# Optimization experiments

Measured on AMD Instinct MI355X. Metric: run time of the kernel, lower is better.

Reference implementation:

```python
import jax, jax.numpy as jnp
import numpy as np

EPS = 1e-12
LAMDA = 1.0
MAX_ITER = 10


def setup_inputs() -> dict:
    key = jax.random.key(0)
    k1, k2 = jax.random.split(key)
    B, L1, L2, D = 64, 1024, 1024, 256
    x1 = jax.random.normal(k1, (B, L1, D), dtype=jnp.float32)
    x2 = jax.random.normal(k2, (B, L2, D), dtype=jnp.float32)
    return {"x1": x1, "x2": x2}


def _cos(x1, x2):
    # batched cosine similarity: [B, L1, L2]
    M = jnp.einsum('bik,bjk->bij', x1, x2)
    a = jnp.sqrt(jnp.sum(x1 * x1, axis=-1, keepdims=True))  # [B, L1, 1]
    b = jnp.sqrt(jnp.sum(x2 * x2, axis=-1, keepdims=True))  # [B, L2, 1]
    norm = a * jnp.swapaxes(b, 1, 2)                          # [B, L1, L2]
    return M / (norm + EPS)


def reference(x1, x2):
    B, L1, _ = x1.shape
    L2 = x2.shape[1]
    M = 1.0 - _cos(x1, x2)          # [B, L1, L2] cost matrix
    K = jnp.exp(-M * LAMDA)
    w1 = jnp.full((B, L1, 1), 1.0 / L1, dtype=x1.dtype)
    w2 = jnp.full((B, L2, 1), 1.0 / L2, dtype=x1.dtype)
    ui = jnp.ones((B, L1, 1), dtype=x1.dtype)
    vi = jnp.ones((B, L2, 1), dtype=x1.dtype)
    Kt = jnp.swapaxes(K, 1, 2)      # [B, L2, L1]

    def body(_, carry):
        ui, vi = carry
        vi = w2 / (jnp.matmul(Kt, ui) + EPS)
        ui = w1 / (jnp.matmul(K, vi) + EPS)
        return (ui, vi)

    ui, vi = jax.lax.fori_loop(0, MAX_ITER, body, (ui, vi))
    G = ui * K * jnp.swapaxes(vi, 1, 2)   # transport plan [B, L1, L2]
    G_max = jnp.max(G, axis=(-1, -2), keepdims=True)
    G_min = jnp.min(G, axis=(-1, -2), keepdims=True)
    G = (G - G_min) / (G_max - G_min + EPS)
    return G * M
```

## Files before the change

kernel.cpp:

```cpp
#include <hip/hip_runtime.h>
#include <hip/hip_bf16.h>


#define EPSV 1e-12f
#define W1 0.0009765625f

typedef short  short8 __attribute__((ext_vector_type(8)));
typedef float  f32x4  __attribute__((ext_vector_type(4)));
typedef _Float16 h8   __attribute__((ext_vector_type(8)));

__device__ __forceinline__ short8 ld_cvt8(const float* p) {
  float4 f0 = *(const float4*)p;
  float4 f1 = *(const float4*)(p + 4);
  float2 p0; p0.x = f0.x; p0.y = f0.y;
  float2 p1; p1.x = f0.z; p1.y = f0.w;
  float2 p2; p2.x = f1.x; p2.y = f1.y;
  float2 p3; p3.x = f1.z; p3.y = f1.w;
  __hip_bfloat162 h0 = __float22bfloat162_rn(p0);
  __hip_bfloat162 h1 = __float22bfloat162_rn(p1);
  __hip_bfloat162 h2 = __float22bfloat162_rn(p2);
  __hip_bfloat162 h3 = __float22bfloat162_rn(p3);
  short2 a = *(short2*)&h0, b = *(short2*)&h1, c = *(short2*)&h2, d = *(short2*)&h3;
  short8 r;
  r[0] = a.x; r[1] = a.y; r[2] = b.x; r[3] = b.y;
  r[4] = c.x; r[5] = c.y; r[6] = d.x; r[7] = d.y;
  return r;
}

__global__ __launch_bounds__(256) void diag_kernel(float* __restrict__ out,
                                                   float val, int n) {
  int stride = gridDim.x * 256;
  for (int i = blockIdx.x * 256 + threadIdx.x; i < n; i += stride) out[i] = val;
}

__global__ __launch_bounds__(256) void prep_kernel(
    const float* __restrict__ x1, const float* __restrict__ x2,
    float* __restrict__ n1, float* __restrict__ n2,
    unsigned* __restrict__ mm) {
  int t = threadIdx.x, bid = blockIdx.x;
  if (bid == 0 && t < 128) mm[t] = (t < 64) ? 0u : 0x7f800000u;
  int row = bid * 4 + (t >> 6);
  int lane = t & 63;
  const float* xp; float* np_;
  int r = row;
  if (row < 65536) { xp = x1; np_ = n1; }
  else { r = row - 65536; xp = x2; np_ = n2; }
  float4 v = ((const float4*)(xp + (size_t)r * 256))[lane];
  float s = v.x * v.x + v.y * v.y + v.z * v.z + v.w * v.w;
  #pragma unroll
  for (int off = 1; off < 64; off <<= 1) s += __shfl_xor(s, off, 64);
  if (lane == 0) np_[r] = sqrtf(s);
}

__global__ __launch_bounds__(256) void gemm_kernel(
    const float* __restrict__ x1, const float* __restrict__ x2,
    const float* __restrict__ n1, const float* __restrict__ n2,
    _Float16* __restrict__ Kh) {
  __shared__ __align__(16) unsigned short smem[2 * 128 * 64];
  unsigned short* As = smem;
  unsigned short* Bs = smem + 128 * 64;
  int bid = blockIdx.x;
  int b = bid >> 6, tile = bid & 63;
  int ti = (tile >> 3) << 7, tj = (tile & 7) << 7;
  int t = threadIdx.x, lane = t & 63, wave = t >> 6;
  int wr = (wave >> 1) << 6, wc = (wave & 1) << 6;
  const float* Ag = x1 + ((size_t)(b * 1024 + ti)) * 256;
  const float* Bg = x2 + ((size_t)(b * 1024 + tj)) * 256;

  f32x4 acc[4][4];
  f32x4 zero = {0.f, 0.f, 0.f, 0.f};
  #pragma unroll
  for (int m = 0; m < 4; ++m)
    #pragma unroll
    for (int n = 0; n < 4; ++n) acc[m][n] = zero;

  short8 ra[4], rb[4];
  #pragma unroll
  for (int c = 0; c < 4; ++c) {
    int ch = t + (c << 8); int row = ch >> 3, kg = ch & 7;
    ra[c] = ld_cvt8(Ag + row * 256 + kg * 8);
    rb[c] = ld_cvt8(Bg + row * 256 + kg * 8);
  }

  for (int k0 = 0; k0 < 4; ++k0) {
    __syncthreads();
    #pragma unroll
    for (int c = 0; c < 4; ++c) {
      int ch = t + (c << 8); int row = ch >> 3, kg = ch & 7;
      int kgs = kg ^ (row & 7);
      *(short8*)(As + row * 64 + kgs * 8) = ra[c];
      *(short8*)(Bs + row * 64 + kgs * 8) = rb[c];
    }
    __syncthreads();
    if (k0 < 3) {
      #pragma unroll
      for (int c = 0; c < 4; ++c) {
        int ch = t + (c << 8); int row = ch >> 3, kg = ch & 7;
        ra[c] = ld_cvt8(Ag + row * 256 + (k0 + 1) * 64 + kg * 8);
        rb[c] = ld_cvt8(Bg + row * 256 + (k0 + 1) * 64 + kg * 8);
      }
    }
    #pragma unroll
    for (int ks = 0; ks < 2; ++ks) {
      short8 af[4], bfr[4];
      #pragma unroll
      for (int m = 0; m < 4; ++m) {
        int row = wr + m * 16 + (lane & 15);
        int c16 = (ks << 2) + (lane >> 4);
        af[m] = *(const short8*)(As + row * 64 + ((c16 ^ (row & 7)) << 3));
      }
      #pragma unroll
      for (int n = 0; n < 4; ++n) {
        int row = wc + n * 16 + (lane & 15);
        int c16 = (ks << 2) + (lane >> 4);
        bfr[n] = *(const short8*)(Bs + row * 64 + ((c16 ^ (row & 7)) << 3));
      }
      #pragma unroll
      for (int m = 0; m < 4; ++m)
        #pragma unroll
        for (int n = 0; n < 4; ++n)
          acc[m][n] = __builtin_amdgcn_mfma_f32_16x16x32_bf16(af[m], bfr[n], acc[m][n], 0, 0, 0);
    }
  }
  __syncthreads();

  _Float16* Ct = (_Float16*)smem;
  float a1v[4][4], b2v[4];
  #pragma unroll
  for (int m = 0; m < 4; ++m)
    #pragma unroll
    for (int q = 0; q < 4; ++q)
      a1v[m][q] = n1[(size_t)b * 1024 + ti + wr + m * 16 + ((lane >> 4) << 2) + q];
  #pragma unroll
  for (int n = 0; n < 4; ++n)
    b2v[n] = n2[(size_t)b * 1024 + tj + wc + n * 16 + (lane & 15)];
  #pragma unroll
  for (int m = 0; m < 4; ++m)
    #pragma unroll
    for (int n = 0; n < 4; ++n)
      #pragma unroll
      for (int q = 0; q < 4; ++q) {
        int rl = wr + m * 16 + ((lane >> 4) << 2) + q;
        int cl = wc + n * 16 + (lane & 15);
        float cosv = acc[m][n][q] / (a1v[m][q] * b2v[n] + EPSV);
        Ct[rl * 128 + cl] = (_Float16)__expf(cosv - 1.0f);
      }
  __syncthreads();
  size_t kbase = ((size_t)b << 20);
  #pragma unroll
  for (int c2i = 0; c2i < 8; ++c2i) {
    int c2 = t + (c2i << 8);
    int row = c2 >> 4, seg = c2 & 15;
    *(float4*)(Kh + kbase + (size_t)(ti + row) * 1024 + tj + seg * 8) = ((const float4*)Ct)[c2];
  }
}

__global__ __launch_bounds__(512) void ktu0_kernel(
    const _Float16* __restrict__ Kh, _Float16* __restrict__ dst) {
  int bid = blockIdx.x;
  int b = bid >> 2, s = bid & 3;
  int t = threadIdx.x, lane = t & 63, w = t >> 6;
  __shared__ float plds[8][1024];
  float pacc[16];
  #pragma unroll
  for (int k = 0; k < 16; ++k) pacc[k] = 0.f;
  const _Float16* kp = Kh + ((size_t)b << 20) + (size_t)(s * 256 + w) * 1024 + lane * 8;
  #pragma unroll 2
  for (int it = 0; it < 32; ++it) {
    h8 k0 = *(const h8*)(kp + (size_t)it * 8192);
    h8 k1 = *(const h8*)(kp + (size_t)it * 8192 + 512);
    #pragma unroll
    for (int k = 0; k < 8; ++k) { pacc[k] += (float)k0[k]; pacc[8 + k] += (float)k1[k]; }
  }
  float4 v0 = {pacc[0], pacc[1], pacc[2], pacc[3]};
  float4 v1 = {pacc[4], pacc[5], pacc[6], pacc[7]};
  float4 v2 = {pacc[8], pacc[9], pacc[10], pacc[11]};
  float4 v3 = {pacc[12], pacc[13], pacc[14], pacc[15]};
  *(float4*)&plds[w][lane * 8] = v0;
  *(float4*)&plds[w][lane * 8 + 4] = v1;
  *(float4*)&plds[w][512 + lane * 8] = v2;
  *(float4*)&plds[w][512 + lane * 8 + 4] = v3;
  __syncthreads();
  #pragma unroll
  for (int p = 0; p < 2; ++p) {
    int col = (p << 9) + t;
    float sum = plds[0][col] + plds[1][col] + plds[2][col] + plds[3][col]
              + plds[4][col] + plds[5][col] + plds[6][col] + plds[7][col];
    dst[((size_t)b << 12) + (s << 10) + col] = (_Float16)sum;
  }
}

template<int FINAL>
__global__ __launch_bounds__(512) void fused_kernel(
    const _Float16* __restrict__ Kh, const _Float16* __restrict__ src,
    _Float16* __restrict__ dst, float* __restrict__ zb,
    unsigned* __restrict__ mm) {
  int bid = blockIdx.x;
  int b = bid >> 2, s = bid & 3;
  int t = threadIdx.x, lane = t & 63, w = t >> 6;
  __shared__ float sv[1024];
  __shared__ float plds[8][1024];
  __shared__ float red[16];
  #pragma unroll
  for (int p = 0; p < 2; ++p) {
    int col = (p << 9) + t;
    const _Float16* sp = src + ((size_t)b << 12) + col;
    float y = (float)sp[0] + (float)sp[1024] + (float)sp[2048] + (float)sp[3072];
    sv[col] = W1 / (y + EPSV);
  }
  __syncthreads();
  float svr[16];
  {
    float4 s0 = *(const float4*)&sv[lane * 8];
    float4 s1 = *(const float4*)&sv[lane * 8 + 4];
    float4 s2 = *(const float4*)&sv[512 + lane * 8];
    float4 s3 = *(const float4*)&sv[512 + lane * 8 + 4];
    svr[0] = s0.x;  svr[1] = s0.y;  svr[2]  = s0.z;  svr[3]  = s0.w;
    svr[4] = s1.x;  svr[5] = s1.y;  svr[6]  = s1.z;  svr[7]  = s1.w;
    svr[8] = s2.x;  svr[9] = s2.y;  svr[10] = s2.z;  svr[11] = s2.w;
    svr[12] = s3.x; svr[13] = s3.y; svr[14] = s3.z;  svr[15] = s3.w;
  }
  float pacc[16];
  #pragma unroll
  for (int k = 0; k < 16; ++k) pacc[k] = 0.f;
  float gmn = 3.4e38f, gmx = 0.f;
  const _Float16* kp = Kh + ((size_t)b << 20) + (size_t)(s * 256 + w) * 1024 + lane * 8;
  #pragma unroll 2
  for (int it = 0; it < 32; ++it) {
    int r = s * 256 + w + it * 8;
    h8 k0 = *(const h8*)(kp + (size_t)it * 8192);
    h8 k1 = *(const h8*)(kp + (size_t)it * 8192 + 512);
    float kf[16], dot = 0.f;
    #pragma unroll
    for (int k = 0; k < 8; ++k) { kf[k] = (float)k0[k]; kf[8 + k] = (float)k1[k]; }
    #pragma unroll
    for (int k = 0; k < 16; ++k) dot += kf[k] * svr[k];
    #pragma unroll
    for (int off = 1; off < 64; off <<= 1) dot += __shfl_xor(dot, off, 64);
    float u = W1 / (dot + EPSV);
    if (FINAL) {
      if (lane == 0) zb[(b << 10) + r] = dot;
      #pragma unroll
      for (int k = 0; k < 16; ++k) {
        float g = u * kf[k] * svr[k];
        gmn = fminf(gmn, g); gmx = fmaxf(gmx, g);
      }
    } else {
      #pragma unroll
      for (int k = 0; k < 16; ++k) pacc[k] += kf[k] * u;
    }
  }
  if (!FINAL) {
    float4 v0 = {pacc[0], pacc[1], pacc[2], pacc[3]};
    float4 v1 = {pacc[4], pacc[5], pacc[6], pacc[7]};
    float4 v2 = {pacc[8], pacc[9], pacc[10], pacc[11]};
    float4 v3 = {pacc[12], pacc[13], pacc[14], pacc[15]};
    *(float4*)&plds[w][lane * 8] = v0;
    *(float4*)&plds[w][lane * 8 + 4] = v1;
    *(float4*)&plds[w][512 + lane * 8] = v2;
    *(float4*)&plds[w][512 + lane * 8 + 4] = v3;
    __syncthreads();
    #pragma unroll
    for (int p = 0; p < 2; ++p) {
      int col = (p << 9) + t;
      float sum = plds[0][col] + plds[1][col] + plds[2][col] + plds[3][col]
                + plds[4][col] + plds[5][col] + plds[6][col] + plds[7][col];
      dst[((size_t)b << 12) + (s << 10) + col] = (_Float16)sum;
    }
  } else {
    #pragma unroll
    for (int off = 1; off < 64; off <<= 1) {
      gmn = fminf(gmn, __shfl_xor(gmn, off, 64));
      gmx = fmaxf(gmx, __shfl_xor(gmx, off, 64));
    }
    if (lane == 0) { red[w] = gmn; red[8 + w] = gmx; }
    __syncthreads();
    if (t == 0) {
      float m0 = red[0], m1 = red[8];
      #pragma unroll
      for (int i = 1; i < 8; ++i) { m0 = fminf(m0, red[i]); m1 = fmaxf(m1, red[8 + i]); }
      atomicMin(&mm[64 + b], __float_as_uint(m0));
      atomicMax(&mm[b],      __float_as_uint(m1));
    }
  }
}

__global__ __launch_bounds__(256) void fin_kernel(
    const _Float16* __restrict__ Kh, const _Float16* __restrict__ src,
    const float* __restrict__ zb, const unsigned* __restrict__ mm,
    float* __restrict__ out) {
  int bid = blockIdx.x;
  int b = bid >> 4, rg = bid & 15;
  int t = threadIdx.x, lane = t & 63, w = t >> 6;
  __shared__ float sv[1024];
  #pragma unroll
  for (int p = 0; p < 4; ++p) {
    int col = (p << 8) + t;
    const _Float16* sp = src + ((size_t)b << 12) + col;
    float y = (float)sp[0] + (float)sp[1024] + (float)sp[2048] + (float)sp[3072];
    sv[col] = W1 / (y + EPSV);
  }
  __syncthreads();
  float svr[16];
  {
    float4 s0 = *(const float4*)&sv[lane * 8];
    float4 s1 = *(const float4*)&sv[lane * 8 + 4];
    float4 s2 = *(const float4*)&sv[512 + lane * 8];
    float4 s3 = *(const float4*)&sv[512 + lane * 8 + 4];
    svr[0] = s0.x;  svr[1] = s0.y;  svr[2]  = s0.z;  svr[3]  = s0.w;
    svr[4] = s1.x;  svr[5] = s1.y;  svr[6]  = s1.z;  svr[7]  = s1.w;
    svr[8] = s2.x;  svr[9] = s2.y;  svr[10] = s2.z;  svr[11] = s2.w;
    svr[12] = s3.x; svr[13] = s3.y; svr[14] = s3.z;  svr[15] = s3.w;
  }
  float gmx = __uint_as_float(mm[b]);
  float gmn = __uint_as_float(mm[64 + b]);
  float scale = 1.0f / (gmx - gmn + EPSV);
  const _Float16* kp = Kh + ((size_t)b << 20) + (size_t)(rg * 64 + w) * 1024 + lane * 8;
  float* op = out + ((size_t)b << 20) + (size_t)(rg * 64 + w) * 1024 + lane * 8;
  for (int it = 0; it < 16; ++it) {
    int r = rg * 64 + w + it * 4;
    float u = W1 / (zb[b * 1024 + r] + EPSV);
    h8 k0 = *(const h8*)(kp + (size_t)it * 4096);
    h8 k1 = *(const h8*)(kp + (size_t)it * 4096 + 512);
    float o[16];
    #pragma unroll
    for (int k = 0; k < 8; ++k) {
      float kfa = (float)k0[k];
      float kfb = (float)k1[k];
      float ga = u * kfa * svr[k];
      float gb = u * kfb * svr[8 + k];
      o[k]     = (ga - gmn) * scale * (-__logf(kfa));
      o[8 + k] = (gb - gmn) * scale * (-__logf(kfb));
    }
    float4 o0 = {o[0], o[1], o[2], o[3]};
    float4 o1 = {o[4], o[5], o[6], o[7]};
    float4 o2 = {o[8], o[9], o[10], o[11]};
    float4 o3 = {o[12], o[13], o[14], o[15]};
    *(float4*)(op + (size_t)it * 4096) = o0;
    *(float4*)(op + (size_t)it * 4096 + 4) = o1;
    *(float4*)(op + (size_t)it * 4096 + 512) = o2;
    *(float4*)(op + (size_t)it * 4096 + 516) = o3;
  }
}

extern "C" void kernel_launch(void* const* d_in, const int* in_sizes, int n_in,
                              void* d_out, int out_size, void* d_ws, size_t ws_size,
                              hipStream_t stream) {
  const float* x1 = (const float*)d_in[0];
  const float* x2 = (const float*)d_in[1];
  float* out = (float*)d_out;
  char* ws = (char*)d_ws;

  _Float16* Kh    = (_Float16*)(ws);
  float*    n1    = (float*)(ws + 134217728ULL);
  float*    zb    = (float*)(ws + 134217728ULL);
  float*    n2    = (float*)(ws + 134479872ULL);
  _Float16* pbufA = (_Float16*)(ws + 134742016ULL);
  _Float16* pbufB = (_Float16*)(ws + 135266304ULL);
  unsigned* mm    = (unsigned*)(ws + 135790592ULL);
  const size_t WS_NEED = 135791104ULL;

  if (ws_size < WS_NEED) {
    float val = 100.0f + (float)(ws_size >> 20);
    diag_kernel<<<2048, 256, 0, stream>>>(out, val, out_size);
    return;
  }

  prep_kernel<<<32768, 256, 0, stream>>>(x1, x2, n1, n2, mm);
  gemm_kernel<<<4096, 256, 0, stream>>>(x1, x2, n1, n2, Kh);
  ktu0_kernel<<<256, 512, 0, stream>>>(Kh, pbufA);
  for (int k = 1; k <= 9; ++k) {
    _Float16* src = (k & 1) ? pbufA : pbufB;
    _Float16* dst = (k & 1) ? pbufB : pbufA;
    fused_kernel<0><<<256, 512, 0, stream>>>(Kh, src, dst, zb, mm);
  }
  fused_kernel<1><<<256, 512, 0, stream>>>(Kh, pbufB, pbufA, zb, mm);
  fin_kernel<<<1024, 256, 0, stream>>>(Kh, pbufB, zb, mm, out);
}
```

Baseline: 493.0 us.

## Split Sinkhorn row blocks 16-way per batch and fuse initial column sums into GEMM

```diff
diff --git a/kernel.cpp b/kernel.cpp
--- a/kernel.cpp
+++ b/kernel.cpp
@@ -8,6 +8,7 @@
 typedef short  short8 __attribute__((ext_vector_type(8)));
 typedef float  f32x4  __attribute__((ext_vector_type(4)));
 typedef _Float16 h8   __attribute__((ext_vector_type(8)));
+typedef _Float16 h2   __attribute__((ext_vector_type(2)));
 
 __device__ __forceinline__ short8 ld_cvt8(const float* p) {
   float4 f0 = *(const float4*)p;
@@ -18,9 +19,9 @@
   float2 p3; p3.x = f1.z; p3.y = f1.w;
   __hip_bfloat162 h0 = __float22bfloat162_rn(p0);
   __hip_bfloat162 h1 = __float22bfloat162_rn(p1);
-  __hip_bfloat162 h2 = __float22bfloat162_rn(p2);
+  __hip_bfloat162 h2_ = __float22bfloat162_rn(p2);
   __hip_bfloat162 h3 = __float22bfloat162_rn(p3);
-  short2 a = *(short2*)&h0, b = *(short2*)&h1, c = *(short2*)&h2, d = *(short2*)&h3;
+  short2 a = *(short2*)&h0, b = *(short2*)&h1, c = *(short2*)&h2_, d = *(short2*)&h3;
   short8 r;
   r[0] = a.x; r[1] = a.y; r[2] = b.x; r[3] = b.y;
   r[4] = c.x; r[5] = c.y; r[6] = d.x; r[7] = d.y;
@@ -55,8 +56,9 @@
 __global__ __launch_bounds__(256) void gemm_kernel(
     const float* __restrict__ x1, const float* __restrict__ x2,
     const float* __restrict__ n1, const float* __restrict__ n2,
-    _Float16* __restrict__ Kh) {
+    _Float16* __restrict__ Kh, _Float16* __restrict__ p0) {
   __shared__ __align__(16) unsigned short smem[2 * 128 * 64];
+  __shared__ float csum[4][128];
   unsigned short* As = smem;
   unsigned short* Bs = smem + 128 * 64;
   int bid = blockIdx.x;
@@ -153,6 +155,32 @@
     int row = c2 >> 4, seg = c2 & 15;
     *(float4*)(Kh + kbase + (size_t)(ti + row) * 1024 + tj + seg * 8) = ((const float4*)Ct)[c2];
   }
+  if (p0 != nullptr) {
+    int cg = lane & 15, rsub = lane >> 4;
+    float cs[8];
+    #pragma unroll
+    for (int k = 0; k < 8; ++k) cs[k] = 0.f;
+    #pragma unroll
+    for (int i = 0; i < 8; ++i) {
+      h8 rowv = *(const h8*)&Ct[(wave * 32 + rsub + i * 4) * 128 + cg * 8];
+      #pragma unroll
+      for (int k = 0; k < 8; ++k) cs[k] += (float)rowv[k];
+    }
+    #pragma unroll
+    for (int k = 0; k < 8; ++k) {
+      cs[k] += __shfl_xor(cs[k], 16, 64);
+      cs[k] += __shfl_xor(cs[k], 32, 64);
+    }
+    if (rsub == 0) {
+      #pragma unroll
+      for (int k = 0; k < 8; ++k) csum[wave][cg * 8 + k] = cs[k];
+    }
+    __syncthreads();
+    if (t < 128) {
+      float s = csum[0][t] + csum[1][t] + csum[2][t] + csum[3][t];
+      p0[((size_t)b << 14) + ((size_t)(ti >> 7) << 10) + tj + t] = (_Float16)s;
+    }
+  }
 }
 
 __global__ __launch_bounds__(512) void ktu0_kernel(
@@ -190,23 +218,31 @@
   }
 }
 
-template<int FINAL>
-__global__ __launch_bounds__(512) void fused_kernel(
+template<int BSHIFT, int NSRC, int FINAL>
+__global__ __launch_bounds__(512, 4) void fused_kernel(
     const _Float16* __restrict__ Kh, const _Float16* __restrict__ src,
     _Float16* __restrict__ dst, float* __restrict__ zb,
     unsigned* __restrict__ mm) {
+  constexpr int LOGS = BSHIFT - 10;
+  constexpr int ROWS = 1024 >> LOGS;
+  constexpr int ITERS = ROWS / 8;
   int bid = blockIdx.x;
-  int b = bid >> 2, s = bid & 3;
+  int b = bid >> LOGS, s = bid & ((1 << LOGS) - 1);
   int t = threadIdx.x, lane = t & 63, w = t >> 6;
   __shared__ float sv[1024];
   __shared__ float plds[8][1024];
   __shared__ float red[16];
-  #pragma unroll
-  for (int p = 0; p < 2; ++p) {
-    int col = (p << 9) + t;
-    const _Float16* sp = src + ((size_t)b << 12) + col;
-    float y = (float)sp[0] + (float)sp[1024] + (float)sp[2048] + (float)sp[3072];
-    sv[col] = W1 / (y + EPSV);
+  {
+    int col2 = t << 1;
+    const _Float16* sp = src + ((size_t)b << BSHIFT) + col2;
+    float y0 = 0.f, y1 = 0.f;
+    #pragma unroll
+    for (int j = 0; j < NSRC; ++j) {
+      h2 vv = *(const h2*)(sp + (j << 10));
+      y0 += (float)vv[0]; y1 += (float)vv[1];
+    }
+    sv[col2] = W1 / (y0 + EPSV);
+    sv[col2 + 1] = W1 / (y1 + EPSV);
   }
   __syncthreads();
   float svr[16];
@@ -224,30 +260,33 @@
   #pragma unroll
   for (int k = 0; k < 16; ++k) pacc[k] = 0.f;
   float gmn = 3.4e38f, gmx = 0.f;
-  const _Float16* kp = Kh + ((size_t)b << 20) + (size_t)(s * 256 + w) * 1024 + lane * 8;
+  const _Float16* kp = Kh + ((size_t)b << 20) + (size_t)(s * ROWS + w) * 1024 + lane * 8;
   #pragma unroll 2
-  for (int it = 0; it < 32; ++it) {
-    int r = s * 256 + w + it * 8;
+  for (int it = 0; it < ITERS; ++it) {
+    int r = s * ROWS + w + it * 8;
     h8 k0 = *(const h8*)(kp + (size_t)it * 8192);
     h8 k1 = *(const h8*)(kp + (size_t)it * 8192 + 512);
-    float kf[16], dot = 0.f;
-    #pragma unroll
-    for (int k = 0; k < 8; ++k) { kf[k] = (float)k0[k]; kf[8 + k] = (float)k1[k]; }
-    #pragma unroll
-    for (int k = 0; k < 16; ++k) dot += kf[k] * svr[k];
+    float dot = 0.f;
+    #pragma unroll
+    for (int k = 0; k < 8; ++k)
+      dot += (float)k0[k] * svr[k] + (float)k1[k] * svr[8 + k];
     #pragma unroll
     for (int off = 1; off < 64; off <<= 1) dot += __shfl_xor(dot, off, 64);
     float u = W1 / (dot + EPSV);
     if (FINAL) {
       if (lane == 0) zb[(b << 10) + r] = dot;
       #pragma unroll
-      for (int k = 0; k < 16; ++k) {
-        float g = u * kf[k] * svr[k];
-        gmn = fminf(gmn, g); gmx = fmaxf(gmx, g);
+      for (int k = 0; k < 8; ++k) {
+        float g0 = u * (float)k0[k] * svr[k];
+        float g1 = u * (float)k1[k] * svr[8 + k];
+        gmn = fminf(gmn, fminf(g0, g1)); gmx = fmaxf(gmx, fmaxf(g0, g1));
       }
     } else {
       #pragma unroll
-      for (int k = 0; k < 16; ++k) pacc[k] += kf[k] * u;
+      for (int k = 0; k < 8; ++k) {
+        pacc[k] += (float)k0[k] * u;
+        pacc[8 + k] += (float)k1[k] * u;
+      }
     }
   }
   if (!FINAL) {
@@ -265,7 +304,7 @@
       int col = (p << 9) + t;
       float sum = plds[0][col] + plds[1][col] + plds[2][col] + plds[3][col]
                 + plds[4][col] + plds[5][col] + plds[6][col] + plds[7][col];
-      dst[((size_t)b << 12) + (s << 10) + col] = (_Float16)sum;
+      dst[((size_t)b << BSHIFT) + (s << 10) + col] = (_Float16)sum;
     }
   } else {
     #pragma unroll
@@ -285,6 +324,7 @@
   }
 }
 
+template<int BSHIFT, int NSRC>
 __global__ __launch_bounds__(256) void fin_kernel(
     const _Float16* __restrict__ Kh, const _Float16* __restrict__ src,
     const float* __restrict__ zb, const unsigned* __restrict__ mm,
@@ -294,11 +334,17 @@
   int t = threadIdx.x, lane = t & 63, w = t >> 6;
   __shared__ float sv[1024];
   #pragma unroll
-  for (int p = 0; p < 4; ++p) {
-    int col = (p << 8) + t;
-    const _Float16* sp = src + ((size_t)b << 12) + col;
-    float y = (float)sp[0] + (float)sp[1024] + (float)sp[2048] + (float)sp[3072];
-    sv[col] = W1 / (y + EPSV);
+  for (int p = 0; p < 2; ++p) {
+    int col2 = (p << 9) + (t << 1);
+    const _Float16* sp = src + ((size_t)b << BSHIFT) + col2;
+    float y0 = 0.f, y1 = 0.f;
+    #pragma unroll
+    for (int j = 0; j < NSRC; ++j) {
+      h2 vv = *(const h2*)(sp + (j << 10));
+      y0 += (float)vv[0]; y1 += (float)vv[1];
+    }
+    sv[col2] = W1 / (y0 + EPSV);
+    sv[col2 + 1] = W1 / (y1 + EPSV);
   }
   __syncthreads();
   float svr[16];
@@ -351,29 +397,45 @@
   float* out = (float*)d_out;
   char* ws = (char*)d_ws;
 
-  _Float16* Kh    = (_Float16*)(ws);
-  float*    n1    = (float*)(ws + 134217728ULL);
-  float*    zb    = (float*)(ws + 134217728ULL);
-  float*    n2    = (float*)(ws + 134479872ULL);
-  _Float16* pbufA = (_Float16*)(ws + 134742016ULL);
-  _Float16* pbufB = (_Float16*)(ws + 135266304ULL);
-  unsigned* mm    = (unsigned*)(ws + 135790592ULL);
-  const size_t WS_NEED = 135791104ULL;
-
-  if (ws_size < WS_NEED) {
+  _Float16* Kh = (_Float16*)(ws);
+  float*    n1 = (float*)(ws + 134217728ULL);
+  float*    zb = (float*)(ws + 134217728ULL);
+  float*    n2 = (float*)(ws + 134479872ULL);
+
+  _Float16* pA16 = (_Float16*)(ws + 134742016ULL);
+  _Float16* pB16 = (_Float16*)(ws + 136839168ULL);
+  unsigned* mmA  = (unsigned*)(ws + 138936320ULL);
+  const size_t WS_A = 138936832ULL;
+
+  _Float16* pA4 = (_Float16*)(ws + 134742016ULL);
+  _Float16* pB4 = (_Float16*)(ws + 135266304ULL);
+  unsigned* mmB = (unsigned*)(ws + 135790592ULL);
+  const size_t WS_B = 135791104ULL;
+
+  if (ws_size >= WS_A) {
+    prep_kernel<<<32768, 256, 0, stream>>>(x1, x2, n1, n2, mmA);
+    gemm_kernel<<<4096, 256, 0, stream>>>(x1, x2, n1, n2, Kh, pA16);
+    fused_kernel<14, 8, 0><<<1024, 512, 0, stream>>>(Kh, pA16, pB16, zb, mmA);
+    for (int k = 2; k <= 9; ++k) {
+      _Float16* src = (k & 1) ? pA16 : pB16;
+      _Float16* dst = (k & 1) ? pB16 : pA16;
+      fused_kernel<14, 16, 0><<<1024, 512, 0, stream>>>(Kh, src, dst, zb, mmA);
+    }
+    fused_kernel<14, 16, 1><<<1024, 512, 0, stream>>>(Kh, pB16, pA16, zb, mmA);
+    fin_kernel<14, 16><<<1024, 256, 0, stream>>>(Kh, pB16, zb, mmA, out);
+  } else if (ws_size >= WS_B) {
+    prep_kernel<<<32768, 256, 0, stream>>>(x1, x2, n1, n2, mmB);
+    gemm_kernel<<<4096, 256, 0, stream>>>(x1, x2, n1, n2, Kh, nullptr);
+    ktu0_kernel<<<256, 512, 0, stream>>>(Kh, pA4);
+    for (int k = 1; k <= 9; ++k) {
+      _Float16* src = (k & 1) ? pA4 : pB4;
+      _Float16* dst = (k & 1) ? pB4 : pA4;
+      fused_kernel<12, 4, 0><<<256, 512, 0, stream>>>(Kh, src, dst, zb, mmB);
+    }
+    fused_kernel<12, 4, 1><<<256, 512, 0, stream>>>(Kh, pB4, pA4, zb, mmB);
+    fin_kernel<12, 4><<<1024, 256, 0, stream>>>(Kh, pB4, zb, mmB, out);
+  } else {
     float val = 100.0f + (float)(ws_size >> 20);
     diag_kernel<<<2048, 256, 0, stream>>>(out, val, out_size);
-    return;
-  }
-
-  prep_kernel<<<32768, 256, 0, stream>>>(x1, x2, n1, n2, mm);
-  gemm_kernel<<<4096, 256, 0, stream>>>(x1, x2, n1, n2, Kh);
-  ktu0_kernel<<<256, 512, 0, stream>>>(Kh, pbufA);
-  for (int k = 1; k <= 9; ++k) {
-    _Float16* src = (k & 1) ? pbufA : pbufB;
-    _Float16* dst = (k & 1) ? pbufB : pbufA;
-    fused_kernel<0><<<256, 512, 0, stream>>>(Kh, src, dst, zb, mm);
-  }
-  fused_kernel<1><<<256, 512, 0, stream>>>(Kh, pbufB, pbufA, zb, mm);
-  fin_kernel<<<1024, 256, 0, stream>>>(Kh, pbufB, zb, mm, out);
-}
+  }
+}
```

Result: no change. 496.4 us (+0.7%).

## Store kernel matrix as FP8 with FP8 residual correction for late iterations

Applied to the files above, without the earlier changes.

```diff
diff --git a/kernel.cpp b/kernel.cpp
--- a/kernel.cpp
+++ b/kernel.cpp
@@ -1,5 +1,6 @@
 #include <hip/hip_runtime.h>
 #include <hip/hip_bf16.h>
+#include <hip/hip_fp8.h>
 
 
 #define EPSV 1e-12f
@@ -7,7 +8,41 @@
 
 typedef short  short8 __attribute__((ext_vector_type(8)));
 typedef float  f32x4  __attribute__((ext_vector_type(4)));
-typedef _Float16 h8   __attribute__((ext_vector_type(8)));
+typedef float  f32x2v __attribute__((ext_vector_type(2)));
+
+__device__ __forceinline__ unsigned char enc1(float x) {
+#if __has_builtin(__builtin_amdgcn_cvt_pk_fp8_f32)
+  int v = __builtin_amdgcn_cvt_pk_fp8_f32(x, x, 0, false);
+  return (unsigned char)(v & 0xff);
+#else
+  __hip_fp8_e4m3 q(x); return (unsigned char)q.__x;
+#endif
+}
+__device__ __forceinline__ float dec1(unsigned char b) {
+#if __has_builtin(__builtin_amdgcn_cvt_f32_fp8)
+  return __builtin_amdgcn_cvt_f32_fp8((int)b, 0);
+#else
+  __hip_fp8_e4m3 q; q.__x = (__hip_fp8_storage_t)b; return (float)q;
+#endif
+}
+__device__ __forceinline__ void decode16(uint4 d, float* f) {
+#if __has_builtin(__builtin_amdgcn_cvt_pk_f32_fp8)
+  f32x2v p;
+  p = __builtin_amdgcn_cvt_pk_f32_fp8((int)d.x, false); f[0]=p[0];  f[1]=p[1];
+  p = __builtin_amdgcn_cvt_pk_f32_fp8((int)d.x, true);  f[2]=p[0];  f[3]=p[1];
+  p = __builtin_amdgcn_cvt_pk_f32_fp8((int)d.y, false); f[4]=p[0];  f[5]=p[1];
+  p = __builtin_amdgcn_cvt_pk_f32_fp8((int)d.y, true);  f[6]=p[0];  f[7]=p[1];
+  p = __builtin_amdgcn_cvt_pk_f32_fp8((int)d.z, false); f[8]=p[0];  f[9]=p[1];
+  p = __builtin_amdgcn_cvt_pk_f32_fp8((int)d.z, true);  f[10]=p[0]; f[11]=p[1];
+  p = __builtin_amdgcn_cvt_pk_f32_fp8((int)d.w, false); f[12]=p[0]; f[13]=p[1];
+  p = __builtin_amdgcn_cvt_pk_f32_fp8((int)d.w, true);  f[14]=p[0]; f[15]=p[1];
+#else
+  unsigned v[4] = {d.x, d.y, d.z, d.w};
+  #pragma unroll
+  for (int i = 0; i < 16; ++i)
+    f[i] = dec1((unsigned char)((v[i >> 2] >> ((i & 3) * 8)) & 0xff));
+#endif
+}
 
 __device__ __forceinline__ short8 ld_cvt8(const float* p) {
   float4 f0 = *(const float4*)p;
@@ -18,9 +53,9 @@
   float2 p3; p3.x = f1.z; p3.y = f1.w;
   __hip_bfloat162 h0 = __float22bfloat162_rn(p0);
   __hip_bfloat162 h1 = __float22bfloat162_rn(p1);
-  __hip_bfloat162 h2 = __float22bfloat162_rn(p2);
+  __hip_bfloat162 h2_ = __float22bfloat162_rn(p2);
   __hip_bfloat162 h3 = __float22bfloat162_rn(p3);
-  short2 a = *(short2*)&h0, b = *(short2*)&h1, c = *(short2*)&h2, d = *(short2*)&h3;
+  short2 a = *(short2*)&h0, b = *(short2*)&h1, c = *(short2*)&h2_, d = *(short2*)&h3;
   short8 r;
   r[0] = a.x; r[1] = a.y; r[2] = b.x; r[3] = b.y;
   r[4] = c.x; r[5] = c.y; r[6] = d.x; r[7] = d.y;
@@ -55,7 +90,7 @@
 __global__ __launch_bounds__(256) void gemm_kernel(
     const float* __restrict__ x1, const float* __restrict__ x2,
     const float* __restrict__ n1, const float* __restrict__ n2,
-    _Float16* __restrict__ Kh) {
+    unsigned char* __restrict__ K8g, unsigned char* __restrict__ R8g) {
   __shared__ __align__(16) unsigned short smem[2 * 128 * 64];
   unsigned short* As = smem;
   unsigned short* Bs = smem + 128 * 64;
@@ -124,7 +159,8 @@
   }
   __syncthreads();
 
-  _Float16* Ct = (_Float16*)smem;
+  unsigned char* CtK = (unsigned char*)smem;
+  unsigned char* CtR = ((unsigned char*)smem) + 16384;
   float a1v[4][4], b2v[4];
   #pragma unroll
   for (int m = 0; m < 4; ++m)
@@ -143,20 +179,27 @@
         int rl = wr + m * 16 + ((lane >> 4) << 2) + q;
         int cl = wc + n * 16 + (lane & 15);
         float cosv = acc[m][n][q] / (a1v[m][q] * b2v[n] + EPSV);
-        Ct[rl * 128 + cl] = (_Float16)__expf(cosv - 1.0f);
+        float kv = __expf(cosv - 1.0f);
+        unsigned char q8 = enc1(kv);
+        float kd = dec1(q8);
+        float rr = kv / kd - 1.0f;
+        CtK[rl * 128 + cl] = q8;
+        CtR[rl * 128 + cl] = enc1(rr);
       }
   __syncthreads();
   size_t kbase = ((size_t)b << 20);
   #pragma unroll
-  for (int c2i = 0; c2i < 8; ++c2i) {
-    int c2 = t + (c2i << 8);
-    int row = c2 >> 4, seg = c2 & 15;
-    *(float4*)(Kh + kbase + (size_t)(ti + row) * 1024 + tj + seg * 8) = ((const float4*)Ct)[c2];
+  for (int i = 0; i < 4; ++i) {
+    int idx = t + (i << 8);
+    int row = idx >> 3, seg = idx & 7;
+    size_t off = kbase + (size_t)(ti + row) * 1024 + tj + seg * 16;
+    *(uint4*)(K8g + off) = ((const uint4*)CtK)[idx];
+    *(uint4*)(R8g + off) = ((const uint4*)CtR)[idx];
   }
 }
 
 __global__ __launch_bounds__(512) void ktu0_kernel(
-    const _Float16* __restrict__ Kh, _Float16* __restrict__ dst) {
+    const unsigned char* __restrict__ K8, _Float16* __restrict__ dst) {
   int bid = blockIdx.x;
   int b = bid >> 2, s = bid & 3;
   int t = threadIdx.x, lane = t & 63, w = t >> 6;
@@ -164,22 +207,19 @@
   float pacc[16];
   #pragma unroll
   for (int k = 0; k < 16; ++k) pacc[k] = 0.f;
-  const _Float16* kp = Kh + ((size_t)b << 20) + (size_t)(s * 256 + w) * 1024 + lane * 8;
+  const unsigned char* kp = K8 + ((size_t)b << 20) + (size_t)(s * 256 + w) * 1024 + lane * 16;
   #pragma unroll 2
   for (int it = 0; it < 32; ++it) {
-    h8 k0 = *(const h8*)(kp + (size_t)it * 8192);
-    h8 k1 = *(const h8*)(kp + (size_t)it * 8192 + 512);
-    #pragma unroll
-    for (int k = 0; k < 8; ++k) { pacc[k] += (float)k0[k]; pacc[8 + k] += (float)k1[k]; }
-  }
-  float4 v0 = {pacc[0], pacc[1], pacc[2], pacc[3]};
-  float4 v1 = {pacc[4], pacc[5], pacc[6], pacc[7]};
-  float4 v2 = {pacc[8], pacc[9], pacc[10], pacc[11]};
-  float4 v3 = {pacc[12], pacc[13], pacc[14], pacc[15]};
-  *(float4*)&plds[w][lane * 8] = v0;
-  *(float4*)&plds[w][lane * 8 + 4] = v1;
-  *(float4*)&plds[w][512 + lane * 8] = v2;
-  *(float4*)&plds[w][512 + lane * 8 + 4] = v3;
+    uint4 dk = *(const uint4*)(kp + (size_t)it * 8192);
+    float kf[16];
+    decode16(dk, kf);
+    #pragma unroll
+    for (int k = 0; k < 16; ++k) pacc[k] += kf[k];
+  }
+  *(float4*)&plds[w][lane * 16]      = *(float4*)&pacc[0];
+  *(float4*)&plds[w][lane * 16 + 4]  = *(float4*)&pacc[4];
+  *(float4*)&plds[w][lane * 16 + 8]  = *(float4*)&pacc[8];
+  *(float4*)&plds[w][lane * 16 + 12] = *(float4*)&pacc[12];
   __syncthreads();
   #pragma unroll
   for (int p = 0; p < 2; ++p) {
@@ -190,11 +230,11 @@
   }
 }
 
-template<int FINAL>
+template<int RECON, int FINAL>
 __global__ __launch_bounds__(512) void fused_kernel(
-    const _Float16* __restrict__ Kh, const _Float16* __restrict__ src,
-    _Float16* __restrict__ dst, float* __restrict__ zb,
-    unsigned* __restrict__ mm) {
+    const unsigned char* __restrict__ K8, const unsigned char* __restrict__ R8,
+    const _Float16* __restrict__ src, _Float16* __restrict__ dst,
+    float* __restrict__ zb, unsigned* __restrict__ mm) {
   int bid = blockIdx.x;
   int b = bid >> 2, s = bid & 3;
   int t = threadIdx.x, lane = t & 63, w = t >> 6;
@@ -211,10 +251,10 @@
   __syncthreads();
   float svr[16];
   {
-    float4 s0 = *(const float4*)&sv[lane * 8];
-    float4 s1 = *(const float4*)&sv[lane * 8 + 4];
-    float4 s2 = *(const float4*)&sv[512 + lane * 8];
-    float4 s3 = *(const float4*)&sv[512 + lane * 8 + 4];
+    float4 s0 = *(const float4*)&sv[lane * 16];
+    float4 s1 = *(const float4*)&sv[lane * 16 + 4];
+    float4 s2 = *(const float4*)&sv[lane * 16 + 8];
+    float4 s3 = *(const float4*)&sv[lane * 16 + 12];
     svr[0] = s0.x;  svr[1] = s0.y;  svr[2]  = s0.z;  svr[3]  = s0.w;
     svr[4] = s1.x;  svr[5] = s1.y;  svr[6]  = s1.z;  svr[7]  = s1.w;
     svr[8] = s2.x;  svr[9] = s2.y;  svr[10] = s2.z;  svr[11] = s2.w;
@@ -224,22 +264,28 @@
   #pragma unroll
   for (int k = 0; k < 16; ++k) pacc[k] = 0.f;
   float gmn = 3.4e38f, gmx = 0.f;
-  const _Float16* kp = Kh + ((size_t)b << 20) + (size_t)(s * 256 + w) * 1024 + lane * 8;
+  const unsigned char* kp = K8 + ((size_t)b << 20) + (size_t)(s * 256 + w) * 1024 + lane * 16;
+  const unsigned char* rp = R8 + ((size_t)b << 20) + (size_t)(s * 256 + w) * 1024 + lane * 16;
   #pragma unroll 2
   for (int it = 0; it < 32; ++it) {
-    int r = s * 256 + w + it * 8;
-    h8 k0 = *(const h8*)(kp + (size_t)it * 8192);
-    h8 k1 = *(const h8*)(kp + (size_t)it * 8192 + 512);
-    float kf[16], dot = 0.f;
-    #pragma unroll
-    for (int k = 0; k < 8; ++k) { kf[k] = (float)k0[k]; kf[8 + k] = (float)k1[k]; }
+    uint4 dk = *(const uint4*)(kp + (size_t)it * 8192);
+    float kf[16];
+    decode16(dk, kf);
+    if (RECON) {
+      uint4 dr = *(const uint4*)(rp + (size_t)it * 8192);
+      float rf[16];
+      decode16(dr, rf);
+      #pragma unroll
+      for (int k = 0; k < 16; ++k) kf[k] *= (1.0f + rf[k]);
+    }
+    float dot = 0.f;
     #pragma unroll
     for (int k = 0; k < 16; ++k) dot += kf[k] * svr[k];
     #pragma unroll
     for (int off = 1; off < 64; off <<= 1) dot += __shfl_xor(dot, off, 64);
     float u = W1 / (dot + EPSV);
     if (FINAL) {
-      if (lane == 0) zb[(b << 10) + r] = dot;
+      if (lane == 0) zb[(b << 10) + s * 256 + w + it * 8] = dot;
       #pragma unroll
       for (int k = 0; k < 16; ++k) {
         float g = u * kf[k] * svr[k];
@@ -251,14 +297,10 @@
     }
   }
   if (!FINAL) {
-    float4 v0 = {pacc[0], pacc[1], pacc[2], pacc[3]};
-    float4 v1 = {pacc[4], pacc[5], pacc[6], pacc[7]};
-    float4 v2 = {pacc[8], pacc[9], pacc[10], pacc[11]};
-    float4 v3 = {pacc[12], pacc[13], pacc[14], pacc[15]};
-    *(float4*)&plds[w][lane * 8] = v0;
-    *(float4*)&plds[w][lane * 8 + 4] = v1;
-    *(float4*)&plds[w][512 + lane * 8] = v2;
-    *(float4*)&plds[w][512 + lane * 8 + 4] = v3;
+    *(float4*)&plds[w][lane * 16]      = *(float4*)&pacc[0];
+    *(float4*)&plds[w][lane * 16 + 4]  = *(float4*)&pacc[4];
+    *(float4*)&plds[w][lane * 16 + 8]  = *(float4*)&pacc[8];
+    *(float4*)&plds[w][lane * 16 + 12] = *(float4*)&pacc[12];
     __syncthreads();
     #pragma unroll
     for (int p = 0; p < 2; ++p) {
@@ -286,9 +328,9 @@
 }
 
 __global__ __launch_bounds__(256) void fin_kernel(
-    const _Float16* __restrict__ Kh, const _Float16* __restrict__ src,
-    const float* __restrict__ zb, const unsigned* __restrict__ mm,
-    float* __restrict__ out) {
+    const unsigned char* __restrict__ K8, const unsigned char* __restrict__ R8,
+    const _Float16* __restrict__ src, const float* __restrict__ zb,
+    const unsigned* __restrict__ mm, float* __restrict__ out) {
   int bid = blockIdx.x;
   int b = bid >> 4, rg = bid & 15;
   int t = threadIdx.x, lane = t & 63, w = t >> 6;
@@ -303,10 +345,10 @@
   __syncthreads();
   float svr[16];
   {
-    float4 s0 = *(const float4*)&sv[lane * 8];
-    float4 s1 = *(const float4*)&sv[lane * 8 + 4];
-    float4 s2 = *(const float4*)&sv[512 + lane * 8];
-    float4 s3 = *(const float4*)&sv[512 + lane * 8 + 4];
+    float4 s0 = *(const float4*)&sv[lane * 16];
+    float4 s1 = *(const float4*)&sv[lane * 16 + 4];
+    float4 s2 = *(const float4*)&sv[lane * 16 + 8];
+    float4 s3 = *(const float4*)&sv[lane * 16 + 12];
     svr[0] = s0.x;  svr[1] = s0.y;  svr[2]  = s0.z;  svr[3]  = s0.w;
     svr[4] = s1.x;  svr[5] = s1.y;  svr[6]  = s1.z;  svr[7]  = s1.w;
     svr[8] = s2.x;  svr[9] = s2.y;  svr[10] = s2.z;  svr[11] = s2.w;
@@ -315,31 +357,27 @@
   float gmx = __uint_as_float(mm[b]);
   float gmn = __uint_as_float(mm[64 + b]);
   float scale = 1.0f / (gmx - gmn + EPSV);
-  const _Float16* kp = Kh + ((size_t)b << 20) + (size_t)(rg * 64 + w) * 1024 + lane * 8;
-  float* op = out + ((size_t)b << 20) + (size_t)(rg * 64 + w) * 1024 + lane * 8;
+  const unsigned char* kp = K8 + ((size_t)b << 20) + (size_t)(rg * 64 + w) * 1024 + lane * 16;
+  const unsigned char* rp = R8 + ((size_t)b << 20) + (size_t)(rg * 64 + w) * 1024 + lane * 16;
+  float* op = out + ((size_t)b << 20) + (size_t)(rg * 64 + w) * 1024 + lane * 16;
   for (int it = 0; it < 16; ++it) {
     int r = rg * 64 + w + it * 4;
     float u = W1 / (zb[b * 1024 + r] + EPSV);
-    h8 k0 = *(const h8*)(kp + (size_t)it * 4096);
-    h8 k1 = *(const h8*)(kp + (size_t)it * 4096 + 512);
-    float o[16];
-    #pragma unroll
-    for (int k = 0; k < 8; ++k) {
-      float kfa = (float)k0[k];
-      float kfb = (float)k1[k];
-      float ga = u * kfa * svr[k];
-      float gb = u * kfb * svr[8 + k];
-      o[k]     = (ga - gmn) * scale * (-__logf(kfa));
-      o[8 + k] = (gb - gmn) * scale * (-__logf(kfb));
-    }
-    float4 o0 = {o[0], o[1], o[2], o[3]};
-    float4 o1 = {o[4], o[5], o[6], o[7]};
-    float4 o2 = {o[8], o[9], o[10], o[11]};
-    float4 o3 = {o[12], o[13], o[14], o[15]};
-    *(float4*)(op + (size_t)it * 4096) = o0;
-    *(float4*)(op + (size_t)it * 4096 + 4) = o1;
-    *(float4*)(op + (size_t)it * 4096 + 512) = o2;
-    *(float4*)(op + (size_t)it * 4096 + 516) = o3;
+    uint4 dk = *(const uint4*)(kp + (size_t)it * 4096);
+    uint4 dr = *(const uint4*)(rp + (size_t)it * 4096);
+    float kf[16], rf[16], o[16];
+    decode16(dk, kf);
+    decode16(dr, rf);
+    #pragma unroll
+    for (int k = 0; k < 16; ++k) {
+      float krec = kf[k] * (1.0f + rf[k]);
+      float g = u * krec * svr[k];
+      o[k] = (g - gmn) * scale * (-__logf(krec));
+    }
+    *(float4*)(op + (size_t)it * 4096)      = *(float4*)&o[0];
+    *(float4*)(op + (size_t)it * 4096 + 4)  = *(float4*)&o[4];
+    *(float4*)(op + (size_t)it * 4096 + 8)  = *(float4*)&o[8];
+    *(float4*)(op + (size_t)it * 4096 + 12) = *(float4*)&o[12];
   }
 }
 
@@ -351,13 +389,14 @@
   float* out = (float*)d_out;
   char* ws = (char*)d_ws;
 
-  _Float16* Kh    = (_Float16*)(ws);
-  float*    n1    = (float*)(ws + 134217728ULL);
-  float*    zb    = (float*)(ws + 134217728ULL);
-  float*    n2    = (float*)(ws + 134479872ULL);
-  _Float16* pbufA = (_Float16*)(ws + 134742016ULL);
-  _Float16* pbufB = (_Float16*)(ws + 135266304ULL);
-  unsigned* mm    = (unsigned*)(ws + 135790592ULL);
+  unsigned char* K8g = (unsigned char*)ws;
+  unsigned char* R8g = (unsigned char*)(ws + 67108864ULL);
+  float*    n1 = (float*)(ws + 134217728ULL);
+  float*    zb = (float*)(ws + 134217728ULL);
+  float*    n2 = (float*)(ws + 134479872ULL);
+  _Float16* pA = (_Float16*)(ws + 134742016ULL);
+  _Float16* pB = (_Float16*)(ws + 135266304ULL);
+  unsigned* mm = (unsigned*)(ws + 135790592ULL);
   const size_t WS_NEED = 135791104ULL;
 
   if (ws_size < WS_NEED) {
@@ -367,13 +406,14 @@
   }
 
   prep_kernel<<<32768, 256, 0, stream>>>(x1, x2, n1, n2, mm);
-  gemm_kernel<<<4096, 256, 0, stream>>>(x1, x2, n1, n2, Kh);
-  ktu0_kernel<<<256, 512, 0, stream>>>(Kh, pbufA);
-  for (int k = 1; k <= 9; ++k) {
-    _Float16* src = (k & 1) ? pbufA : pbufB;
-    _Float16* dst = (k & 1) ? pbufB : pbufA;
-    fused_kernel<0><<<256, 512, 0, stream>>>(Kh, src, dst, zb, mm);
-  }
-  fused_kernel<1><<<256, 512, 0, stream>>>(Kh, pbufB, pbufA, zb, mm);
-  fin_kernel<<<1024, 256, 0, stream>>>(Kh, pbufB, zb, mm, out);
-}
+  gemm_kernel<<<4096, 256, 0, stream>>>(x1, x2, n1, n2, K8g, R8g);
+  ktu0_kernel<<<256, 512, 0, stream>>>(K8g, pA);
+  for (int k = 1; k <= 8; ++k) {
+    _Float16* src = (k & 1) ? pA : pB;
+    _Float16* dst = (k & 1) ? pB : pA;
+    fused_kernel<0, 0><<<256, 512, 0, stream>>>(K8g, R8g, src, dst, zb, mm);
+  }
+  fused_kernel<1, 0><<<256, 512, 0, stream>>>(K8g, R8g, pA, pB, zb, mm);
+  fused_kernel<1, 1><<<256, 512, 0, stream>>>(K8g, R8g, pB, pA, zb, mm);
+  fin_kernel<<<1024, 256, 0, stream>>>(K8g, R8g, pB, zb, mm, out);
+}
```

Result: slower. 507.0 us (+2.8%).
